# Optimization experiments

Measured on AMD Instinct MI355X. Metric: run time of the kernel, lower is better.

Reference implementation:

```python
import jax, jax.numpy as jnp
import numpy as np

STRIDE = 1  # conv stride from __init__


def setup_inputs() -> dict:
    key = jax.random.key(0)
    k1, k2, k3 = jax.random.split(key, 3)
    prot1 = jax.random.normal(k1, (4, 1024, 8, 64), dtype=jnp.float32)
    prot2 = jax.random.normal(k2, (4, 1024, 8, 64), dtype=jnp.float32)
    # W: (no_filters, no_channels, no_dims, window_size)
    W = jax.random.normal(k3, (32, 8, 64, 7), dtype=jnp.float32)
    return {"prot1": prot1, "prot2": prot2, "W": W}


def _project(x, W, stride):
    """Fused equivalent of unfold + broadcast-mul + sum over (C, window).

    x: (N, H, C, D), W: (F, C, D, w) -> (N, F, H', D) with H' = (H - w)//stride + 1.
    This is a grouped 1D conv: D groups, each mixing C input channels into F outputs.
    """
    N, H, C, D = x.shape
    Fn, _, _, w = W.shape
    xg = jnp.transpose(x, (0, 3, 2, 1)).reshape(N, D * C, H)        # (N, D*C, H)
    Wg = jnp.transpose(W, (2, 0, 1, 3)).reshape(D * Fn, C, w)       # (D*F, C, w)
    out = jax.lax.conv_general_dilated(
        xg, Wg, window_strides=(stride,), padding='VALID',
        dimension_numbers=('NCH', 'OIH', 'NCH'), feature_group_count=D)
    Hp = out.shape[-1]
    return jnp.transpose(out.reshape(N, D, Fn, Hp), (0, 2, 3, 1))   # (N, F, H', D)


def reference(prot1, prot2, W):
    q1 = _project(prot1, W, STRIDE)   # (N, F, H1', D)
    q2 = _project(prot2, W, STRIDE)   # (N, F, H2', D)
    H1p, H2p = q1.shape[2], q2.shape[2]
    scale = jnp.sqrt(jnp.asarray(H1p * H2p, dtype=q1.dtype))
    att = jnp.einsum('nfhd,nfgd->nfhg', q1, q2) / scale             # (N, F, H1', H2')
    a = jax.nn.softmax(att, axis=3)
    p1 = jnp.einsum('nfhg,nfgd->nfhd', a, q2)                       # (N, F, H1', D)
    # NB: source does transpose(att, 2, 2) (a no-op) and multiplies the SAME
    # softmax matrix by the UPDATED p1folds; we reproduce that faithfully.
    p2 = jnp.einsum('nfhg,nfgd->nfhd', a, p1)                       # (N, F, H1', D)
    out1 = jnp.tanh(jnp.transpose(p1, (0, 2, 1, 3)))                # (N, H1', F, D)
    out2 = jnp.tanh(jnp.transpose(p2, (0, 2, 1, 3)))
    # Dropout is identity in eval mode (and dropout_p=0.0 here).
    return (out1, out2)
```

## Files before the change

### kernel.cpp

```cpp
#include <hip/hip_runtime.h>
#include <math.h>

typedef __bf16 bf16_t;
typedef bf16_t bf16x4 __attribute__((ext_vector_type(4)));
typedef bf16_t bf16x8 __attribute__((ext_vector_type(8)));
typedef float  f32x16 __attribute__((ext_vector_type(16)));

#define HH 1024
#define CC 8
#define DD 64
#define FF 32
#define WW 7
#define HP 1018
#define HPAD 1024
#define NF 128
#define QOUT (NF*HP*DD)
#define QWS ((size_t)NF*HPAD*DD)

#if __has_builtin(__builtin_amdgcn_exp2f)
#define EXP2(x) __builtin_amdgcn_exp2f(x)
#else
#define EXP2(x) __expf((x) * 0.6931471805599453f)
#endif

#define QSCALE (1.442695040888963f / 1018.f)

__device__ __forceinline__ int vaddr(int row, int col) {
    return row*64 + ((((col>>3) ^ (row&7) ^ ((row>>2)&7)))<<3) + (col&7);
}

__global__ __launch_bounds__(256) void wprep_kernel(
    const float* __restrict__ Wt, float* __restrict__ Wp)
{
    const int idx = blockIdx.x * 256 + threadIdx.x;
    if (idx < FF*CC*DD*WW) {
        const int j = idx % WW;
        int t = idx / WW;
        const int d = t % DD; t /= DD;
        const int c = t % CC;
        const int f = t / CC;
        Wp[((f*CC + c)*WW + j)*DD + d] = Wt[idx];
    }
}

__global__ __launch_bounds__(256, 3) void conv_kernel(
    const float* __restrict__ x1, const float* __restrict__ x2,
    const float* __restrict__ Wp, bf16_t* __restrict__ q1, bf16_t* __restrict__ q2)
{
    __shared__ float xs[22*512];
    const int zin = blockIdx.z & 1;
    const int fh = blockIdx.z >> 1;
    const float* x = zin ? x2 : x1;
    bf16_t* q = zin ? q2 : q1;
    const float qs = zin ? 1.f : QSCALE;
    const int n = blockIdx.y;
    const int hb = blockIdx.x * 16;
    const int tid = threadIdx.x;

    const float4* xg = (const float4*)(x + (size_t)n*HH*512);
    float4* xsv = (float4*)xs;
#pragma unroll
    for (int it = 0; it < 11; ++it) {
        const int i = it*256 + tid;
        const int row = hb + (i >> 7);
        float4 v = {0.f, 0.f, 0.f, 0.f};
        if (row < HH) v = xg[(size_t)row*128 + (i & 127)];
        xsv[i] = v;
    }

    const int d = tid & 63;
    const int fq = tid >> 6;

    float w[2][CC][WW];
#pragma unroll
    for (int fi = 0; fi < 2; ++fi) {
        const int f = fq*8 + fh*2 + fi;
#pragma unroll
        for (int c = 0; c < CC; ++c)
#pragma unroll
            for (int j = 0; j < WW; ++j)
                w[fi][c][j] = Wp[((f*CC + c)*WW + j)*DD + d];
    }

    __syncthreads();

    float acc[2][16];
#pragma unroll
    for (int fi = 0; fi < 2; ++fi)
#pragma unroll
        for (int i = 0; i < 16; ++i) acc[fi][i] = 0.f;

#pragma unroll
    for (int rr = 0; rr < 22; ++rr) {
        float xv[CC];
#pragma unroll
        for (int c = 0; c < CC; ++c)
            xv[c] = xs[rr*512 + c*64 + d];
#pragma unroll
        for (int fi = 0; fi < 2; ++fi)
#pragma unroll
            for (int j = 0; j < WW; ++j) {
                const int i = rr - j;
                if (i >= 0 && i < 16) {
#pragma unroll
                    for (int c = 0; c < CC; ++c)
                        acc[fi][i] = fmaf(xv[c], w[fi][c][j], acc[fi][i]);
                }
            }
    }

#pragma unroll
    for (int fi = 0; fi < 2; ++fi) {
        const int f = fq*8 + fh*2 + fi;
#pragma unroll
        for (int i = 0; i < 16; ++i) {
            const int h = hb + i;
            const float v = (h < HP) ? acc[fi][i]*qs : 0.f;
            q[((size_t)(n*FF + f)*HPAD + h)*DD + d] = (bf16_t)v;
        }
    }
}

__device__ __forceinline__ float fast_tanh(float x) {
    const float t = __expf(2.f * x);
    return (t - 1.f) / (t + 1.f);
}

template<int MODE>
__global__ __launch_bounds__(256, 2) void flash(
    const bf16_t* __restrict__ q1, const bf16_t* __restrict__ q2,
    const bf16_t* __restrict__ vsrc, bf16_t* __restrict__ p1out,
    float* __restrict__ out)
{
    __shared__ __align__(16) bf16_t Vt[2][64*64];

    const int head = blockIdx.y;
    const int n = head >> 5, f = head & 31;
    const int tid = threadIdx.x;
    const int w = tid >> 6;
    const int lane = tid & 63;
    const int lid = lane & 31;
    const int half = lane >> 5;
    const int hb = blockIdx.x * 256 + w * 64;

    const size_t qoff = (size_t)head * HPAD * DD;
    const int vswz = (lid & 7) ^ (lid >> 2);

    const int gq = tid >> 4;
    const int dq = tid & 15;
    const int cgb = 4*((gq>>1)&1) + 8*(gq&1) + 16*(gq>>2);

    const bf16_t* vptr = (MODE == 1) ? vsrc : q2;

    const bf16_t* bp = q1 + qoff + (size_t)(hb + lid)*DD + 8*half;
    const bf16_t* ap = q2 + qoff + (size_t)lid*DD + 8*half;
    const bf16_t* vp = vptr + qoff + (size_t)(4*gq)*DD + 4*dq;

    bf16x8 bq1[2][4];
#pragma unroll
    for (int nt = 0; nt < 2; ++nt)
#pragma unroll
        for (int kt = 0; kt < 4; ++kt)
            bq1[nt][kt] = *(const bf16x8*)&bp[(size_t)(32*nt)*DD + 16*kt];

    bf16x8 aq[2][4];
#pragma unroll
    for (int mt = 0; mt < 2; ++mt)
#pragma unroll
        for (int kt = 0; kt < 4; ++kt)
            aq[mt][kt] = *(const bf16x8*)&ap[(size_t)(32*mt)*DD + 16*kt];

    bf16x4 rV[4];
#pragma unroll
    for (int i = 0; i < 4; ++i)
        rV[i] = *(const bf16x4*)&vp[(size_t)i*DD];
#pragma unroll
    for (int j = 0; j < 4; ++j) {
        bf16x4 c = { rV[0][j], rV[1][j], rV[2][j], rV[3][j] };
        *(bf16x4*)&Vt[0][vaddr(4*dq + j, cgb)] = c;
    }
#pragma unroll
    for (int i = 0; i < 4; ++i)
        rV[i] = *(const bf16x4*)&vp[(size_t)(64 + i)*DD];

    f32x16 O[2][2] = {};
    float lacc[2] = {0.f, 0.f};

    __syncthreads();

    for (int t = 0; t < 16; ++t) {
        const int g0 = t << 6;
        const bf16_t* vtc = Vt[t & 1];

        if (t + 1 < 16) {
            bf16_t* vtn = Vt[(t + 1) & 1];
#pragma unroll
            for (int j = 0; j < 4; ++j) {
                bf16x4 c = { rV[0][j], rV[1][j], rV[2][j], rV[3][j] };
                *(bf16x4*)&vtn[vaddr(4*dq + j, cgb)] = c;
            }
            if (t + 2 < 16) {
#pragma unroll
                for (int i = 0; i < 4; ++i)
                    rV[i] = *(const bf16x4*)&vp[(size_t)((t + 2)*64 + i)*DD];
            }
        }

        const bool tail = (g0 + 64 > HP);

#pragma unroll
        for (int mt = 0; mt < 2; ++mt) {
            f32x16 C[2] = {};
            __builtin_amdgcn_s_setprio(1);
#pragma unroll
            for (int kt = 0; kt < 4; ++kt) {
                C[0] = __builtin_amdgcn_mfma_f32_32x32x16_bf16(aq[mt][kt], bq1[0][kt], C[0], 0,0,0);
                C[1] = __builtin_amdgcn_mfma_f32_32x32x16_bf16(aq[mt][kt], bq1[1][kt], C[1], 0,0,0);
            }
            __builtin_amdgcn_s_setprio(0);
            if (g0 + 64 < HPAD) {
#pragma unroll
                for (int kt = 0; kt < 4; ++kt)
                    aq[mt][kt] = *(const bf16x8*)&ap[(size_t)(g0 + 64 + 32*mt)*DD + 16*kt];
            }
            bf16x8 af[2][2];
#pragma unroll
            for (int nt = 0; nt < 2; ++nt) {
                float ls = 0.f;
#pragma unroll
                for (int s = 0; s < 16; ++s) {
                    float e = EXP2(C[nt][s]);
                    if (tail) {
                        const int gg = g0 + 32*mt + (s&3) + 8*(s>>2) + 4*half;
                        if (gg >= HP) e = 0.f;
                    }
                    ls += e;
                    af[nt][s>>3][s&7] = (bf16_t)e;
                }
                lacc[nt] += ls;
            }
            __builtin_amdgcn_s_setprio(1);
#pragma unroll
            for (int u = 0; u < 2; ++u) {
#pragma unroll
                for (int dt = 0; dt < 2; ++dt) {
                    const int chunk = (4*mt + 2*u + half) ^ vswz;
                    bf16x8 b = *(const bf16x8*)&vtc[(32*dt + lid)*64 + chunk*8];
                    O[0][dt] = __builtin_amdgcn_mfma_f32_32x32x16_bf16(af[0][u], b, O[0][dt], 0,0,0);
                    O[1][dt] = __builtin_amdgcn_mfma_f32_32x32x16_bf16(af[1][u], b, O[1][dt], 0,0,0);
                }
            }
            __builtin_amdgcn_s_setprio(0);
        }
        __syncthreads();
    }

    float linv[2];
#pragma unroll
    for (int nt = 0; nt < 2; ++nt) {
        const float l = lacc[nt] + __shfl_xor(lacc[nt], 32);
        linv[nt] = 1.f / l;
    }
#pragma unroll
    for (int ht = 0; ht < 2; ++ht) {
#pragma unroll
        for (int s = 0; s < 16; ++s) {
            const int R = (s&3) + 8*(s>>2) + 4*half;
            const float li = __shfl(linv[ht], R);
            const int hg = hb + 32*ht + R;
#pragma unroll
            for (int dt = 0; dt < 2; ++dt) {
                const int d = 32*dt + lid;
                const float val = O[ht][dt][s] * li;
                if (hg < HP)
                    out[(((size_t)n*HP + hg)*FF + f)*DD + d] = fast_tanh(val);
                if (MODE == 0)
                    p1out[qoff + (size_t)hg*DD + d] = (bf16_t)(hg < HP ? val : 0.f);
            }
        }
    }
}

extern "C" void kernel_launch(void* const* d_in, const int* in_sizes, int n_in,
                              void* d_out, int out_size, void* d_ws, size_t ws_size,
                              hipStream_t stream)
{
    const float* prot1 = (const float*)d_in[0];
    const float* prot2 = (const float*)d_in[1];
    const float* Wt    = (const float*)d_in[2];
    float* out = (float*)d_out;

    bf16_t* q1b = (bf16_t*)d_ws;
    bf16_t* q2b = q1b + QWS;
    bf16_t* p1b = q2b + QWS;
    float* Wp   = (float*)(p1b + QWS);

    wprep_kernel<<<dim3(448), 256, 0, stream>>>(Wt, Wp);
    conv_kernel<<<dim3(64, 4, 8), 256, 0, stream>>>(prot1, prot2, Wp, q1b, q2b);
    flash<0><<<dim3(4, NF), 256, 0, stream>>>(q1b, q2b, q2b, p1b, out);
    flash<1><<<dim3(4, NF), 256, 0, stream>>>(q1b, q2b, p1b, p1b, out + QOUT);
}
```

Baseline: 207.9 us.

## Software-pipeline QK^T MFMA with exp/PV of previous subtile in flash loop

Restructures the attention inner loop so the S=QK^T MFMAs for the next 32-row subtile are issued before the exp and PV work of the current subtile. Two score buffers (CA, CB) ping-pong, and the first S phase is hoisted before the loop. The goal is to overlap MFMA latency with the transcendental exp work and the LDS reads instead of running them back to back. This raises register pressure from the extra 32-float accumulator set, which under launch_bounds(256,2) could cause spills.

New measurement: 209.1 us. Within noise of the previous version (+0.6%).

```diff
diff --git a/kernel.cpp b/kernel.cpp
--- a/kernel.cpp
+++ b/kernel.cpp
@@ -126,6 +126,48 @@
     return (t - 1.f) / (t + 1.f);
 }
 
+#define S_PHASE(Cd, aqm) {                                                        \
+    f32x16 _z{};                                                                  \
+    Cd[0] = _z; Cd[1] = _z;                                                       \
+    __builtin_amdgcn_s_setprio(1);                                                \
+    _Pragma("unroll")                                                             \
+    for (int kt = 0; kt < 4; ++kt) {                                              \
+        Cd[0] = __builtin_amdgcn_mfma_f32_32x32x16_bf16(aqm[kt], bq1[0][kt], Cd[0], 0,0,0); \
+        Cd[1] = __builtin_amdgcn_mfma_f32_32x32x16_bf16(aqm[kt], bq1[1][kt], Cd[1], 0,0,0); \
+    }                                                                             \
+    __builtin_amdgcn_s_setprio(0); }
+
+#define EXP_PHASE(Cs, af, mtv) {                                                  \
+    _Pragma("unroll")                                                             \
+    for (int nt = 0; nt < 2; ++nt) {                                              \
+        float ls = 0.f;                                                           \
+        _Pragma("unroll")                                                         \
+        for (int s = 0; s < 16; ++s) {                                            \
+            float e = EXP2(Cs[nt][s]);                                            \
+            if (tail) {                                                           \
+                const int gg = g0 + 32*(mtv) + (s&3) + 8*(s>>2) + 4*half;         \
+                if (gg >= HP) e = 0.f;                                            \
+            }                                                                     \
+            ls += e;                                                              \
+            af[nt][s>>3][s&7] = (bf16_t)e;                                        \
+        }                                                                         \
+        lacc[nt] += ls;                                                           \
+    } }
+
+#define PV_PHASE(af, mtv) {                                                       \
+    __builtin_amdgcn_s_setprio(1);                                                \
+    _Pragma("unroll")                                                             \
+    for (int u = 0; u < 2; ++u) {                                                 \
+        _Pragma("unroll")                                                         \
+        for (int dt = 0; dt < 2; ++dt) {                                          \
+            const int chunk = (4*(mtv) + 2*u + half) ^ vswz;                      \
+            bf16x8 b = *(const bf16x8*)&vtc[(32*dt + lid)*64 + chunk*8];          \
+            O[0][dt] = __builtin_amdgcn_mfma_f32_32x32x16_bf16(af[0][u], b, O[0][dt], 0,0,0); \
+            O[1][dt] = __builtin_amdgcn_mfma_f32_32x32x16_bf16(af[1][u], b, O[1][dt], 0,0,0); \
+        }                                                                         \
+    }                                                                             \
+    __builtin_amdgcn_s_setprio(0); }
+
 template<int MODE>
 __global__ __launch_bounds__(256, 2) void flash(
     const bf16_t* __restrict__ q1, const bf16_t* __restrict__ q2,
@@ -186,11 +228,18 @@
     f32x16 O[2][2] = {};
     float lacc[2] = {0.f, 0.f};
 
+    f32x16 CA[2], CB[2];
+    S_PHASE(CA, aq[0]);
+#pragma unroll
+    for (int kt = 0; kt < 4; ++kt)
+        aq[0][kt] = *(const bf16x8*)&ap[(size_t)64*DD + 16*kt];
+
     __syncthreads();
 
     for (int t = 0; t < 16; ++t) {
         const int g0 = t << 6;
         const bf16_t* vtc = Vt[t & 1];
+        const bool tail = (t == 15);
 
         if (t + 1 < 16) {
             bf16_t* vtn = Vt[(t + 1) & 1];
@@ -206,52 +255,32 @@
             }
         }
 
-        const bool tail = (g0 + 64 > HP);
-
-#pragma unroll
-        for (int mt = 0; mt < 2; ++mt) {
-            f32x16 C[2] = {};
-            __builtin_amdgcn_s_setprio(1);
-#pragma unroll
-            for (int kt = 0; kt < 4; ++kt) {
-                C[0] = __builtin_amdgcn_mfma_f32_32x32x16_bf16(aq[mt][kt], bq1[0][kt], C[0], 0,0,0);
-                C[1] = __builtin_amdgcn_mfma_f32_32x32x16_bf16(aq[mt][kt], bq1[1][kt], C[1], 0,0,0);
-            }
-            __builtin_amdgcn_s_setprio(0);
-            if (g0 + 64 < HPAD) {
+        S_PHASE(CB, aq[1]);
+        if (t + 1 < 16) {
+#pragma unroll
+            for (int kt = 0; kt < 4; ++kt)
+                aq[1][kt] = *(const bf16x8*)&ap[(size_t)((t + 1)*64 + 32)*DD + 16*kt];
+        }
+        {
+            bf16x8 af[2][2];
+            EXP_PHASE(CA, af, 0);
+            PV_PHASE(af, 0);
+        }
+
+        if (t + 1 < 16) {
+            S_PHASE(CA, aq[0]);
+            if (t + 2 < 16) {
 #pragma unroll
                 for (int kt = 0; kt < 4; ++kt)
-                    aq[mt][kt] = *(const bf16x8*)&ap[(size_t)(g0 + 64 + 32*mt)*DD + 16*kt];
-            }
+                    aq[0][kt] = *(const bf16x8*)&ap[(size_t)((t + 2)*64)*DD + 16*kt];
+            }
+        }
+        {
             bf16x8 af[2][2];
-#pragma unroll
-            for (int nt = 0; nt < 2; ++nt) {
-                float ls = 0.f;
-#pragma unroll
-                for (int s = 0; s < 16; ++s) {
-                    float e = EXP2(C[nt][s]);
-                    if (tail) {
-                        const int gg = g0 + 32*mt + (s&3) + 8*(s>>2) + 4*half;
-                        if (gg >= HP) e = 0.f;
-                    }
-                    ls += e;
-                    af[nt][s>>3][s&7] = (bf16_t)e;
-                }
-                lacc[nt] += ls;
-            }
-            __builtin_amdgcn_s_setprio(1);
-#pragma unroll
-            for (int u = 0; u < 2; ++u) {
-#pragma unroll
-                for (int dt = 0; dt < 2; ++dt) {
-                    const int chunk = (4*mt + 2*u + half) ^ vswz;
-                    bf16x8 b = *(const bf16x8*)&vtc[(32*dt + lid)*64 + chunk*8];
-                    O[0][dt] = __builtin_amdgcn_mfma_f32_32x32x16_bf16(af[0][u], b, O[0][dt], 0,0,0);
-                    O[1][dt] = __builtin_amdgcn_mfma_f32_32x32x16_bf16(af[1][u], b, O[1][dt], 0,0,0);
-                }
-            }
-            __builtin_amdgcn_s_setprio(0);
-        }
+            EXP_PHASE(CB, af, 1);
+            PV_PHASE(af, 1);
+        }
+
         __syncthreads();
     }
 
```

## Split flash attention work across 8 waves with 32 query rows each

Applied to the files above, without the earlier changes.

The flash kernel now launches 512 threads per block, with each wave handling 32 query rows instead of 64. This halves the per-wave accumulator and QK register footprint and raises occupancy bounds to 4 blocks. Only the first 256 threads stage V into shared memory. In exchange, each wave reloads the K tiles (q2) independently, so global and L2 traffic for K per output row doubles, and the MFMA reuse of each A fragment drops.

Result: slower. 810.5 us (+289.8%).

```diff
diff --git a/kernel.cpp b/kernel.cpp
--- a/kernel.cpp
+++ b/kernel.cpp
@@ -127,7 +127,7 @@
 }
 
 template<int MODE>
-__global__ __launch_bounds__(256, 2) void flash(
+__global__ __launch_bounds__(512, 4) void flash(
     const bf16_t* __restrict__ q1, const bf16_t* __restrict__ q2,
     const bf16_t* __restrict__ vsrc, bf16_t* __restrict__ p1out,
     float* __restrict__ out)
@@ -141,12 +141,13 @@
     const int lane = tid & 63;
     const int lid = lane & 31;
     const int half = lane >> 5;
-    const int hb = blockIdx.x * 256 + w * 64;
+    const int hb = blockIdx.x * 256 + w * 32;
 
     const size_t qoff = (size_t)head * HPAD * DD;
     const int vswz = (lid & 7) ^ (lid >> 2);
 
-    const int gq = tid >> 4;
+    const bool stg = (tid < 256);
+    const int gq = (tid & 255) >> 4;
     const int dq = tid & 15;
     const int cgb = 4*((gq>>1)&1) + 8*(gq&1) + 16*(gq>>2);
 
@@ -156,12 +157,10 @@
     const bf16_t* ap = q2 + qoff + (size_t)lid*DD + 8*half;
     const bf16_t* vp = vptr + qoff + (size_t)(4*gq)*DD + 4*dq;
 
-    bf16x8 bq1[2][4];
-#pragma unroll
-    for (int nt = 0; nt < 2; ++nt)
-#pragma unroll
-        for (int kt = 0; kt < 4; ++kt)
-            bq1[nt][kt] = *(const bf16x8*)&bp[(size_t)(32*nt)*DD + 16*kt];
+    bf16x8 bq1[4];
+#pragma unroll
+    for (int kt = 0; kt < 4; ++kt)
+        bq1[kt] = *(const bf16x8*)&bp[16*kt];
 
     bf16x8 aq[2][4];
 #pragma unroll
@@ -171,28 +170,31 @@
             aq[mt][kt] = *(const bf16x8*)&ap[(size_t)(32*mt)*DD + 16*kt];
 
     bf16x4 rV[4];
-#pragma unroll
-    for (int i = 0; i < 4; ++i)
-        rV[i] = *(const bf16x4*)&vp[(size_t)i*DD];
-#pragma unroll
-    for (int j = 0; j < 4; ++j) {
-        bf16x4 c = { rV[0][j], rV[1][j], rV[2][j], rV[3][j] };
-        *(bf16x4*)&Vt[0][vaddr(4*dq + j, cgb)] = c;
-    }
-#pragma unroll
-    for (int i = 0; i < 4; ++i)
-        rV[i] = *(const bf16x4*)&vp[(size_t)(64 + i)*DD];
-
-    f32x16 O[2][2] = {};
-    float lacc[2] = {0.f, 0.f};
+    if (stg) {
+#pragma unroll
+        for (int i = 0; i < 4; ++i)
+            rV[i] = *(const bf16x4*)&vp[(size_t)i*DD];
+#pragma unroll
+        for (int j = 0; j < 4; ++j) {
+            bf16x4 c = { rV[0][j], rV[1][j], rV[2][j], rV[3][j] };
+            *(bf16x4*)&Vt[0][vaddr(4*dq + j, cgb)] = c;
+        }
+#pragma unroll
+        for (int i = 0; i < 4; ++i)
+            rV[i] = *(const bf16x4*)&vp[(size_t)(64 + i)*DD];
+    }
+
+    f32x16 O[2] = {};
+    float lacc = 0.f;
 
     __syncthreads();
 
     for (int t = 0; t < 16; ++t) {
         const int g0 = t << 6;
         const bf16_t* vtc = Vt[t & 1];
-
-        if (t + 1 < 16) {
+        const bool tail = (t == 15);
+
+        if (stg && t + 1 < 16) {
             bf16_t* vtn = Vt[(t + 1) & 1];
 #pragma unroll
             for (int j = 0; j < 4; ++j) {
@@ -206,39 +208,32 @@
             }
         }
 
-        const bool tail = (g0 + 64 > HP);
-
 #pragma unroll
         for (int mt = 0; mt < 2; ++mt) {
-            f32x16 C[2] = {};
+            f32x16 C = {};
             __builtin_amdgcn_s_setprio(1);
 #pragma unroll
-            for (int kt = 0; kt < 4; ++kt) {
-                C[0] = __builtin_amdgcn_mfma_f32_32x32x16_bf16(aq[mt][kt], bq1[0][kt], C[0], 0,0,0);
-                C[1] = __builtin_amdgcn_mfma_f32_32x32x16_bf16(aq[mt][kt], bq1[1][kt], C[1], 0,0,0);
-            }
+            for (int kt = 0; kt < 4; ++kt)
+                C = __builtin_amdgcn_mfma_f32_32x32x16_bf16(aq[mt][kt], bq1[kt], C, 0,0,0);
             __builtin_amdgcn_s_setprio(0);
-            if (g0 + 64 < HPAD) {
+            if (t + 1 < 16) {
 #pragma unroll
                 for (int kt = 0; kt < 4; ++kt)
-                    aq[mt][kt] = *(const bf16x8*)&ap[(size_t)(g0 + 64 + 32*mt)*DD + 16*kt];
-            }
-            bf16x8 af[2][2];
-#pragma unroll
-            for (int nt = 0; nt < 2; ++nt) {
-                float ls = 0.f;
-#pragma unroll
-                for (int s = 0; s < 16; ++s) {
-                    float e = EXP2(C[nt][s]);
-                    if (tail) {
-                        const int gg = g0 + 32*mt + (s&3) + 8*(s>>2) + 4*half;
-                        if (gg >= HP) e = 0.f;
-                    }
-                    ls += e;
-                    af[nt][s>>3][s&7] = (bf16_t)e;
+                    aq[mt][kt] = *(const bf16x8*)&ap[(size_t)((t + 1)*64 + 32*mt)*DD + 16*kt];
+            }
+            bf16x8 af[2];
+            float ls = 0.f;
+#pragma unroll
+            for (int s = 0; s < 16; ++s) {
+                float e = EXP2(C[s]);
+                if (tail) {
+                    const int gg = g0 + 32*mt + (s&3) + 8*(s>>2) + 4*half;
+                    if (gg >= HP) e = 0.f;
                 }
-                lacc[nt] += ls;
-            }
+                ls += e;
+                af[s>>3][s&7] = (bf16_t)e;
+            }
+            lacc += ls;
             __builtin_amdgcn_s_setprio(1);
 #pragma unroll
             for (int u = 0; u < 2; ++u) {
@@ -246,8 +241,7 @@
                 for (int dt = 0; dt < 2; ++dt) {
                     const int chunk = (4*mt + 2*u + half) ^ vswz;
                     bf16x8 b = *(const bf16x8*)&vtc[(32*dt + lid)*64 + chunk*8];
-                    O[0][dt] = __builtin_amdgcn_mfma_f32_32x32x16_bf16(af[0][u], b, O[0][dt], 0,0,0);
-                    O[1][dt] = __builtin_amdgcn_mfma_f32_32x32x16_bf16(af[1][u], b, O[1][dt], 0,0,0);
+                    O[dt] = __builtin_amdgcn_mfma_f32_32x32x16_bf16(af[u], b, O[dt], 0,0,0);
                 }
             }
             __builtin_amdgcn_s_setprio(0);
@@ -255,28 +249,21 @@
         __syncthreads();
     }
 
-    float linv[2];
-#pragma unroll
-    for (int nt = 0; nt < 2; ++nt) {
-        const float l = lacc[nt] + __shfl_xor(lacc[nt], 32);
-        linv[nt] = 1.f / l;
-    }
-#pragma unroll
-    for (int ht = 0; ht < 2; ++ht) {
-#pragma unroll
-        for (int s = 0; s < 16; ++s) {
-            const int R = (s&3) + 8*(s>>2) + 4*half;
-            const float li = __shfl(linv[ht], R);
-            const int hg = hb + 32*ht + R;
-#pragma unroll
-            for (int dt = 0; dt < 2; ++dt) {
-                const int d = 32*dt + lid;
-                const float val = O[ht][dt][s] * li;
-                if (hg < HP)
-                    out[(((size_t)n*HP + hg)*FF + f)*DD + d] = fast_tanh(val);
-                if (MODE == 0)
-                    p1out[qoff + (size_t)hg*DD + d] = (bf16_t)(hg < HP ? val : 0.f);
-            }
+    const float l = lacc + __shfl_xor(lacc, 32);
+    const float linv = 1.f / l;
+#pragma unroll
+    for (int s = 0; s < 16; ++s) {
+        const int R = (s&3) + 8*(s>>2) + 4*half;
+        const float li = __shfl(linv, R);
+        const int hg = hb + R;
+#pragma unroll
+        for (int dt = 0; dt < 2; ++dt) {
+            const int d = 32*dt + lid;
+            const float val = O[dt][s] * li;
+            if (hg < HP)
+                out[(((size_t)n*HP + hg)*FF + f)*DD + d] = fast_tanh(val);
+            if (MODE == 0)
+                p1out[qoff + (size_t)hg*DD + d] = (bf16_t)(hg < HP ? val : 0.f);
         }
     }
 }
@@ -297,6 +284,6 @@
 
     wprep_kernel<<<dim3(448), 256, 0, stream>>>(Wt, Wp);
     conv_kernel<<<dim3(64, 4, 8), 256, 0, stream>>>(prot1, prot2, Wp, q1b, q2b);
-    flash<0><<<dim3(4, NF), 256, 0, stream>>>(q1b, q2b, q2b, p1b, out);
-    flash<1><<<dim3(4, NF), 256, 0, stream>>>(q1b, q2b, p1b, p1b, out + QOUT);
-}
+    flash<0><<<dim3(4, NF), 512, 0, stream>>>(q1b, q2b, q2b, p1b, out);
+    flash<1><<<dim3(4, NF), 512, 0, stream>>>(q1b, q2b, p1b, p1b, out + QOUT);
+}
```
